# Kernel optimization log

Measured on AMD Instinct MI355X. Metric: run time of the kernel, lower is better.

## Reference

```python
import jax, jax.numpy as jnp
import numpy as np

SCALE = 256.0  # emulates SharedFxpShift = 8 fixed-point shift


def requant(x):
    # RequantFxpToScaledInt8: shift down by SharedFxpShift and clamp to int8 range
    return jnp.clip(x / SCALE, -128.0, 127.0)


def prelu(x, a):
    return jnp.where(x >= 0, x, a * x)


def _linearize(c):
    # injective encoding of 3D int coords (coords in [-8, 2040) after +8 shift)
    c = c.astype(jnp.int64) + 8
    B = 2048
    return (c[:, 0] * B + c[:, 1]) * B + c[:, 2]


def sparse_conv(coords, feats, W, stride):
    # 3x3x3 submanifold sparse conv: for each kernel offset, hash-lookup the
    # neighbor via sorted linearized coords + searchsorted, gather, matmul.
    # coords [N,3] int32, feats [N,Cin], W [27,Cin,Cout]
    lin = _linearize(coords)
    perm = jnp.argsort(lin)
    slin = lin[perm]
    N = coords.shape[0]
    out = jnp.zeros((N, W.shape[-1]), feats.dtype)
    k = 0
    for dx in (-1, 0, 1):
        for dy in (-1, 0, 1):
            for dz in (-1, 0, 1):
                off = jnp.array([dx, dy, dz], jnp.int32) * stride
                q = _linearize(coords + off[None, :])
                pos = jnp.clip(jnp.searchsorted(slin, q), 0, N - 1)
                hit = slin[pos] == q
                nb = perm[pos]
                f = jnp.where(hit[:, None], feats[nb], 0.0)
                out = out + f @ W[k]
                k += 1
    return out


def setup_inputs() -> dict:
    N, M, C = 200000, 400000, 64
    rng = np.random.default_rng(0)
    # unique parent coords: multiples of 2 in 512^3 grid
    lin = rng.choice(2 ** 24, size=N, replace=False).astype(np.int64)
    px = (lin // (256 * 256)) % 256
    py = (lin // 256) % 256
    pz = lin % 256
    rec_C = (np.stack([px, py, pz], 1) * 2).astype(np.int32)  # [N,3], stride 2
    # exactly M occupied children out of N*8, sorted (row-major mask order)
    child_idx = np.sort(rng.choice(N * 8, size=M, replace=False)).astype(np.int32)
    parent = child_idx // 8
    bit = child_idx % 8
    off = np.stack([(bit >> 2) & 1, (bit >> 1) & 1, bit & 1], 1).astype(np.int32)
    child_C = rec_C[parent] + off  # [M,3], stride 1, unique
    bins1_bits = np.zeros((N, 8), np.int32)
    bins1_bits[parent, bit] = 1
    bins0_bits = rng.integers(0, 2, size=(M, 8)).astype(np.int32)

    key = jax.random.key(0)
    ks = jax.random.split(key, 20)

    def w(k, shape, fan_in):
        return jax.random.normal(k, shape, jnp.float32) / np.sqrt(fan_in)

    inp = {
        "rec_F": jax.random.normal(ks[0], (N, C), jnp.float32) * SCALE,
        "dec_W": w(ks[1], (C + 8, C), C + 8),
        "dec_b": w(ks[2], (C,), 1) * 0.1,
        "dec_a": jnp.full((C,), 0.25, jnp.float32),
        "res_W1": w(ks[3], (27, C, C), 27 * C),
        "res_b1": w(ks[4], (C,), 1) * 0.1,
        "res_a1": jnp.full((C,), 0.25, jnp.float32),
        "res_W2": w(ks[5], (27, C, C), 27 * C),
        "res_b2": w(ks[6], (C,), 1) * 0.1,
        "p0_Wc": w(ks[7], (27, C, C), 27 * C),
        "p0_bc": w(ks[8], (C,), 1) * 0.1,
        "p0_ac": jnp.full((C,), 0.25, jnp.float32),
        "p0_Wl": w(ks[9], (C, C * 8), C),
        "p1_Wc": w(ks[10], (27, C, C), 27 * C),
        "p1_bc": w(ks[11], (C,), 1) * 0.1,
        "p1_ac": jnp.full((C,), 0.25, jnp.float32),
        "p1_Wl": w(ks[12], (C, 255), C),
        "rec_C": jnp.asarray(rec_C),
        "bins1_bits": jnp.asarray(bins1_bits),
        "child_idx": jnp.asarray(child_idx),
        "child_C": jnp.asarray(child_C),
        "bins0_bits": jnp.asarray(bins0_bits),
    }
    return inp


def reference(rec_F, dec_W, dec_b, dec_a, res_W1, res_b1, res_a1, res_W2, res_b2,
              p0_Wc, p0_bc, p0_ac, p0_Wl, p1_Wc, p1_bc, p1_ac, p1_Wl,
              rec_C, bins1_bits, child_idx, child_C, bins0_bits):
    C = dec_W.shape[1]
    # embed (empty Sequential for pred_steps=2): bins1.F << SharedFxpShift
    embed_f = bins1_bits.astype(jnp.float32) * SCALE  # [N,8]
    x = jnp.concatenate([rec_F, embed_f], 1)  # [N, C+8]
    # dec: Requant -> LinearPReLU(C+8 -> C, out32) -> ResBlock(C)
    h = requant(x)
    h = prelu(h @ dec_W + dec_b, dec_a)  # [N,C]
    r = requant(h)
    r = prelu(sparse_conv(rec_C, r, res_W1, 2) + res_b1, res_a1)
    r = requant(r)
    r = sparse_conv(rec_C, r, res_W2, 2) + res_b2
    rec_out = h + r  # [N,C]
    # pred[0]: Requant -> SparseConvPReLU(out8) -> Linear(C -> 8C, out32)
    p = requant(rec_out)
    p = requant(prelu(sparse_conv(rec_C, p, p0_Wc, 2) + p0_bc, p0_ac))
    p = p @ p0_Wl  # [N, 8C]
    # boolean-mask gather of occupied children: reshape [N,8,C] then mask ->
    # equals flat row gather with precomputed sorted child indices
    p = p.reshape(-1, C)[child_idx]  # [M,C]
    # pred[1] (last): Requant -> SparseConvPReLU(out8) -> Linear(C -> 255, out32)
    p = requant(p)
    p = requant(prelu(sparse_conv(child_C, p, p1_Wc, 1) + p1_bc, p1_ac))
    pred_out = p @ p1_Wl  # [M,255]
    # cur_oct = (cur_bins[0].F << bin2oct_kernel).sum(1) - 1
    k = jnp.arange(8, dtype=jnp.int32)
    cur_oct = ((bins0_bits << k).sum(1) - 1).astype(jnp.int16)  # [M]
    return rec_out, pred_out, cur_oct
```

## Files before the change

kernel.cpp:

```cpp
#include <hip/hip_runtime.h>
#include <stdint.h>


typedef short bf16x8 __attribute__((ext_vector_type(8)));
typedef float f32x4 __attribute__((ext_vector_type(4)));

#define EMPTY_KEY 0xFFFFFFFFu

__device__ __forceinline__ float rq(float x) {
  x *= (1.0f / 256.0f);
  return fminf(fmaxf(x, -128.0f), 127.0f);
}

__device__ __forceinline__ short f2b(float f) {
  union { float f; uint32_t u; } v; v.f = f;
  uint32_t u = v.u;
  uint32_t r = (u + 0x7FFFu + ((u >> 16) & 1u)) >> 16;
  return (short)r;
}

__device__ __forceinline__ uint32_t hkey(int x, int y, int z) {
  return ((uint32_t)(x + 8) << 20) | ((uint32_t)(y + 8) << 10) | (uint32_t)(z + 8);
}
__device__ __forceinline__ uint32_t hfun(uint32_t key, uint32_t mask) {
  return (key * 2654435761u) & mask;
}


__device__ __forceinline__ void pack_conv_elem(const float* __restrict__ W,
                                               short* __restrict__ dst, int gid) {
  int lane = gid & 63;
  int c = (gid >> 6) & 3;
  int t = (gid >> 8) & 1;
  int k = gid >> 9;
  int n = c * 16 + (lane & 15);
  int g = lane >> 4;
  bf16x8 v;
#pragma unroll
  for (int e = 0; e < 8; e++) {
    int kk = t * 32 + g * 8 + e;
    v[e] = f2b(W[(k * 64 + kk) * 64 + n]);
  }
  *(bf16x8*)(dst + gid * 8) = v;
}

__device__ __forceinline__ void pack_dense_elem(const float* __restrict__ W,
                                                short* __restrict__ dst, int K,
                                                int Ncols, int KT, int CT, int gid) {
  if (gid >= KT * CT * 64) return;
  int lane = gid & 63;
  int c = (gid >> 6) % CT;
  int t = gid / (64 * CT);
  int n = c * 16 + (lane & 15);
  int g = lane >> 4;
  bf16x8 v;
#pragma unroll
  for (int e = 0; e < 8; e++) {
    int kk = t * 32 + g * 8 + e;
    float val = (kk < K && n < Ncols) ? W[kk * Ncols + n] : 0.0f;
    v[e] = f2b(val);
  }
  *(bf16x8*)(dst + gid * 8) = v;
}

struct SetupA {
  const float *dec_W, *p0_Wl, *p1_Wl, *res_W1, *res_W2, *p0_Wc, *p1_Wc;
  const int *bins1, *child_idx, *bins0;
  uint32_t* rkeys;
  short *wpack, *decwp, *p0wp, *p1wp;
  int *bitsPk, *pStart, *bcnt;
  float* outOct;
  int N, M;
};

__global__ void __launch_bounds__(256) k_setupA(SetupA s) {
  int bid = blockIdx.x, tid = threadIdx.x;
  if (bid < 2048) {
    s.rkeys[bid * 256 + tid] = EMPTY_KEY;
    return;
  }
  bid -= 2048;
  if (bid < 216) {
    int which = bid / 54, sb = bid % 54;
    int gid = sb * 256 + tid;
    if (gid < 27 * 2 * 4 * 64) {
      const float* W = which == 0 ? s.res_W1 : which == 1 ? s.res_W2
                     : which == 2 ? s.p0_Wc : s.p1_Wc;
      pack_conv_elem(W, s.wpack + which * 110592, gid);
    }
    return;
  }
  bid -= 216;
  if (bid < 27) {
    if (bid < 3) pack_dense_elem(s.dec_W, s.decwp, 72, 64, 3, 4, bid * 256 + tid);
    else if (bid < 19) pack_dense_elem(s.p0_Wl, s.p0wp, 64, 512, 2, 32, (bid - 3) * 256 + tid);
    else pack_dense_elem(s.p1_Wl, s.p1wp, 64, 255, 2, 16, (bid - 19) * 256 + tid);
    return;
  }
  bid -= 27;
  int nbN = (s.N + 255) / 256, nbM = (s.M + 255) / 256;
  if (bid < nbN) {
    int p = bid * 256 + tid;
    if (p < s.N) {
      int b = 0;
#pragma unroll
      for (int e = 0; e < 8; e++) b |= (s.bins1[(size_t)p * 8 + e] & 1) << e;
      s.bitsPk[p] = b;
    }
    return;
  }
  bid -= nbN;
  if (bid < nbM) {
    int m = bid * 256 + tid;
    if (m < s.M) {
      int p = s.child_idx[m] >> 3;
      if (m == 0 || (s.child_idx[m - 1] >> 3) != p) s.pStart[p] = m;
    }
    return;
  }
  bid -= nbM;
  if (bid < nbM) {
    int m = bid * 256 + tid;
    if (m < s.M) {
      int ss = 0;
#pragma unroll
      for (int e = 0; e < 8; e++) ss += s.bins0[(size_t)m * 8 + e] << e;
      s.outOct[m] = (float)(ss - 1);
    }
    return;
  }
  if (tid < 8) s.bcnt[tid] = 0;
}

__global__ void __launch_bounds__(256)
k_setupB(const int* __restrict__ rec_C, const int* __restrict__ child_idx,
         uint32_t* __restrict__ rkeys, int* __restrict__ rvals,
         int* __restrict__ lists, int* __restrict__ cnt, int N, int M) {
  int bid = blockIdx.x, tid = threadIdx.x;
  int nbN = (N + 255) / 256;
  if (bid < nbN) {
    int i = bid * 256 + tid;
    if (i >= N) return;
    uint32_t key = hkey(rec_C[i * 3], rec_C[i * 3 + 1], rec_C[i * 3 + 2]);
    uint32_t s = hfun(key, (1u << 19) - 1);
    while (true) {
      uint32_t old = atomicCAS(&rkeys[s], EMPTY_KEY, key);
      if (old == EMPTY_KEY) { rvals[s] = i; return; }
      s = (s + 1) & ((1u << 19) - 1);
    }
  }
  bid -= nbN;
  __shared__ int lcnt[8];
  __shared__ int lbase[8];
  if (tid < 8) lcnt[tid] = 0;
  __syncthreads();
  int m = bid * 256 + tid;
  int b = 0, lp = 0;
  if (m < M) {
    b = child_idx[m] & 7;
    lp = atomicAdd(&lcnt[b], 1);
  }
  __syncthreads();
  if (tid < 8) lbase[tid] = atomicAdd(&cnt[tid], lcnt[tid]);
  __syncthreads();
  if (m < M) lists[(size_t)b * M + lbase[b] + lp] = m;
}

__global__ void __launch_bounds__(256)
k_setupC1(const int* __restrict__ rec_C,
          const uint32_t* __restrict__ rkeys, const int* __restrict__ rvals,
          int* __restrict__ nbrR, int N) {
  const uint32_t rmask = (1u << 19) - 1;
  int t = blockIdx.x * 256 + threadIdx.x;
  if (t >= N * 27) return;
  int i = t / 27, k = t % 27;
  int dx = k / 9 - 1, dy = (k / 3) % 3 - 1, dz = k % 3 - 1;
  int x = rec_C[i * 3] + dx * 2;
  int y = rec_C[i * 3 + 1] + dy * 2;
  int z = rec_C[i * 3 + 2] + dz * 2;
  uint32_t key = hkey(x, y, z);
  uint32_t s = hfun(key, rmask);
  int res = -1;
  while (true) {
    uint32_t kk = rkeys[s];
    if (kk == key) { res = rvals[s]; break; }
    if (kk == EMPTY_KEY) break;
    s = (s + 1) & rmask;
  }
  nbrR[(size_t)i * 28 + k] = res;
}

__global__ void __launch_bounds__(256)
k_setupC2(const int* __restrict__ child_C, const int* __restrict__ child_idx,
          const int* __restrict__ nbrR, const int* __restrict__ bitsPacked,
          const int* __restrict__ parentStart, int* __restrict__ nbrC, int M) {
  int m = blockIdx.x * 256 + threadIdx.x;
  if (m >= M) return;
  int cx = child_C[(size_t)m * 3], cy = child_C[(size_t)m * 3 + 1],
      cz = child_C[(size_t)m * 3 + 2];
  int pr = child_idx[m] >> 3;
  const int* nrow = nbrR + (size_t)pr * 28;
  int px = cx & 1, py = cy & 1, pz = cz & 1;

  int b8[8], s8[8];
#pragma unroll
  for (int j = 0; j < 8; j++) {
    int ddx = (px - 1) + ((j >> 2) & 1);
    int ddy = (py - 1) + ((j >> 1) & 1);
    int ddz = (pz - 1) + (j & 1);
    int kk = (ddx + 1) * 9 + (ddy + 1) * 3 + (ddz + 1);
    int r = nrow[kk];
    b8[j] = (r >= 0) ? bitsPacked[r] : 0;
    s8[j] = (r >= 0) ? parentStart[r] : 0;
  }

  int nout[28];
  nout[27] = -1;
#pragma unroll
  for (int k = 0; k < 27; k++) {
    const int dx = k / 9 - 1, dy = (k / 3) % 3 - 1, dz = k % 3 - 1;
    int tx = cx + dx, ty = cy + dy, tz = cz + dz;
    int jx = ((px + dx + 2) >> 1) - px;
    int jy = ((py + dy + 2) >> 1) - py;
    int jz = ((pz + dz + 2) >> 1) - pz;
    int j = jx * 4 + jy * 2 + jz;
    int bit = ((tx & 1) << 2) | ((ty & 1) << 1) | (tz & 1);
    int bits = b8[j];
    int res = -1;
    if ((bits >> bit) & 1) res = s8[j] + __popc(bits & ((1 << bit) - 1));
    nout[k] = res;
  }
#pragma unroll
  for (int q = 0; q < 7; q++)
    *(int4*)(nbrC + (size_t)m * 28 + q * 4) =
        make_int4(nout[q * 4], nout[q * 4 + 1], nout[q * 4 + 2], nout[q * 4 + 3]);
}


__global__ void __launch_bounds__(256)
k_dec(const float* __restrict__ recF, const int* __restrict__ bits,
      const short* __restrict__ wp, const float* __restrict__ bias,
      const float* __restrict__ alpha, float* __restrict__ h32,
      short* __restrict__ hq) {
  int tid = threadIdx.x, wid = tid >> 6, lane = tid & 63;
  int rowbase = blockIdx.x * 64 + wid * 16;
  int lrow = rowbase + (lane & 15);
  int g = lane >> 4;
  f32x4 acc[4] = {};
#pragma unroll
  for (int t = 0; t < 3; t++) {
    bf16x8 a = {0, 0, 0, 0, 0, 0, 0, 0};
    if (t < 2) {
      const float* src = recF + (size_t)lrow * 64 + t * 32 + g * 8;
#pragma unroll
      for (int e = 0; e < 8; e++) a[e] = f2b(rq(src[e]));
    } else if (g == 0) {
      const int* bp = bits + (size_t)lrow * 8;
#pragma unroll
      for (int e = 0; e < 8; e++) a[e] = f2b((float)bp[e]);
    }
#pragma unroll
    for (int c = 0; c < 4; c++) {
      bf16x8 b = *(const bf16x8*)(wp + ((t * 4 + c) * 64 + lane) * 8);
      acc[c] = __builtin_amdgcn_mfma_f32_16x16x32_bf16(a, b, acc[c], 0, 0, 0);
    }
  }
#pragma unroll
  for (int c = 0; c < 4; c++) {
    int col = c * 16 + (lane & 15);
    float bi = bias[col], al = alpha[col];
#pragma unroll
    for (int r = 0; r < 4; r++) {
      int row = rowbase + g * 4 + r;
      float v = acc[c][r] + bi;
      v = v >= 0.0f ? v : al * v;
      h32[(size_t)row * 64 + col] = v;
      hq[(size_t)row * 64 + col] = f2b(rq(v));
    }
  }
}

template <int MODE>
__global__ void __launch_bounds__(256)
k_conv(const short* __restrict__ fin, const int* __restrict__ nbr,
       const short* __restrict__ wp, const float* __restrict__ bias,
       const float* __restrict__ alpha, const float* __restrict__ resid,
       float* __restrict__ out32, short* __restrict__ outq) {
  int tid = threadIdx.x, wid = tid >> 6, lane = tid & 63;
  int rowbase = blockIdx.x * 64 + wid * 16;
  int lrow = rowbase + (lane & 15);
  int g = lane >> 4;

  int4 nv[7];
#pragma unroll
  for (int j = 0; j < 7; j++)
    nv[j] = *(const int4*)(nbr + (size_t)lrow * 28 + j * 4);
  int nbk[28];
#pragma unroll
  for (int j = 0; j < 7; j++) {
    nbk[j * 4 + 0] = nv[j].x;
    nbk[j * 4 + 1] = nv[j].y;
    nbk[j * 4 + 2] = nv[j].z;
    nbk[j * 4 + 3] = nv[j].w;
  }

  const bf16x8 zz = {0, 0, 0, 0, 0, 0, 0, 0};
  f32x4 acc[4] = {};
#pragma unroll
  for (int k = 0; k < 27; k++) {
    if (__any(nbk[k] >= 0)) {
      int nb = nbk[k];
      int safe = nb >= 0 ? nb : 0;
      const short* fp = fin + (size_t)safe * 64 + g * 8;
      bf16x8 a0 = *(const bf16x8*)fp;
      bf16x8 a1 = *(const bf16x8*)(fp + 32);
      a0 = nb >= 0 ? a0 : zz;
      a1 = nb >= 0 ? a1 : zz;
      const short* wk = wp + k * 4096;
#pragma unroll
      for (int c = 0; c < 4; c++) {
        bf16x8 b0 = *(const bf16x8*)(wk + (c * 64 + lane) * 8);
        acc[c] = __builtin_amdgcn_mfma_f32_16x16x32_bf16(a0, b0, acc[c], 0, 0, 0);
      }
#pragma unroll
      for (int c = 0; c < 4; c++) {
        bf16x8 b1 = *(const bf16x8*)(wk + ((4 + c) * 64 + lane) * 8);
        acc[c] = __builtin_amdgcn_mfma_f32_16x16x32_bf16(a1, b1, acc[c], 0, 0, 0);
      }
    }
  }
#pragma unroll
  for (int c = 0; c < 4; c++) {
    int col = c * 16 + (lane & 15);
    float bi = bias[col];
    float al = (MODE == 0) ? alpha[col] : 0.0f;
#pragma unroll
    for (int r = 0; r < 4; r++) {
      int row = rowbase + g * 4 + r;
      float v = acc[c][r] + bi;
      if (MODE == 0) {
        v = v >= 0.0f ? v : al * v;
        outq[(size_t)row * 64 + col] = f2b(rq(v));
      } else {
        v += resid[(size_t)row * 64 + col];
        out32[(size_t)row * 64 + col] = v;
        outq[(size_t)row * 64 + col] = f2b(rq(v));
      }
    }
  }
}

__global__ void __launch_bounds__(256)
k_p0(const short* __restrict__ qq, const int* __restrict__ child_idx,
     const int* __restrict__ lists, const int* __restrict__ cnt,
     const short* __restrict__ wp, short* __restrict__ tq, int M) {
  int b = blockIdx.y;
  int cb = cnt[b];
  int start = blockIdx.x * 64;
  if (start >= cb) return;
  int tid = threadIdx.x, wid = tid >> 6, lane = tid & 63, g = lane >> 4;
  int posA = start + wid * 16 + (lane & 15);
  int parent = -1;
  if (posA < cb) parent = child_idx[lists[(size_t)b * M + posA]] >> 3;
  f32x4 acc[4] = {};
#pragma unroll
  for (int t = 0; t < 2; t++) {
    bf16x8 a = {0, 0, 0, 0, 0, 0, 0, 0};
    if (parent >= 0) a = *(const bf16x8*)(qq + (size_t)parent * 64 + t * 32 + g * 8);
#pragma unroll
    for (int c = 0; c < 4; c++) {
      bf16x8 bb = *(const bf16x8*)(wp + (((size_t)t * 32 + b * 4 + c) * 64 + lane) * 8);
      acc[c] = __builtin_amdgcn_mfma_f32_16x16x32_bf16(a, bb, acc[c], 0, 0, 0);
    }
  }
#pragma unroll
  for (int r = 0; r < 4; r++) {
    int posD = start + wid * 16 + g * 4 + r;
    if (posD < cb) {
      int m = lists[(size_t)b * M + posD];
#pragma unroll
      for (int c = 0; c < 4; c++) {
        int col = c * 16 + (lane & 15);
        tq[(size_t)m * 64 + col] = f2b(rq(acc[c][r]));
      }
    }
  }
}

__global__ void __launch_bounds__(256, 4)
k_convp1(const short* __restrict__ fin, const int* __restrict__ nbr,
         const short* __restrict__ wp, const float* __restrict__ bias,
         const float* __restrict__ alpha,
         const int* __restrict__ lists, const int* __restrict__ cnt,
         const short* __restrict__ p1wp, float* __restrict__ out, int M) {
  __shared__ short lds[4][16][64];
  __shared__ int mrow[4][16];
  int b = blockIdx.y;
  int cb = cnt[b];
  int start = blockIdx.x * 64;
  if (start >= cb) return;
  int tid = threadIdx.x, wid = tid >> 6, lane = tid & 63;
  int l15 = lane & 15, g = lane >> 4;

  int pos = start + wid * 16 + l15;
  int m = (pos < cb) ? lists[(size_t)b * M + pos] : -1;
  if (g == 0) mrow[wid][l15] = m;

  int msafe = m >= 0 ? m : 0;
  const int* nrow = nbr + (size_t)msafe * 28;

  int px = (b >> 2) & 1, py = (b >> 1) & 1, pz = b & 1;
  int kown[8];
  uint32_t ownMask = 0;
#pragma unroll
  for (int j = 0; j < 8; j++) {
    int k = (((j >> 2) & 1) - px + 1) * 9 + (((j >> 1) & 1) - py + 1) * 3 +
            ((j & 1) - pz + 1);
    kown[j] = k;
    ownMask |= 1u << k;
  }

  int nbo[8];
#pragma unroll
  for (int j = 0; j < 8; j++) nbo[j] = nrow[kown[j]];
  int4 nv[7];
#pragma unroll
  for (int j = 0; j < 7; j++) nv[j] = *(const int4*)(nrow + j * 4);
  __builtin_amdgcn_sched_barrier(0);

  const bf16x8 zz = {0, 0, 0, 0, 0, 0, 0, 0};

  bf16x8 A0[8], A1[8];
#pragma unroll
  for (int j = 0; j < 8; j++) {
    int nb = (m >= 0) ? nbo[j] : -1;
    int safe = nb >= 0 ? nb : 0;
    const short* fp = fin + (size_t)safe * 64 + g * 8;
    bf16x8 x0 = *(const bf16x8*)fp;
    bf16x8 x1 = *(const bf16x8*)(fp + 32);
    A0[j] = nb >= 0 ? x0 : zz;
    A1[j] = nb >= 0 ? x1 : zz;
  }
  __builtin_amdgcn_sched_barrier(0);

  f32x4 acc[4] = {};
#pragma unroll
  for (int j = 0; j < 8; j++) {
    const short* wk = wp + kown[j] * 4096;
#pragma unroll
    for (int c = 0; c < 4; c++) {
      bf16x8 b0 = *(const bf16x8*)(wk + (c * 64 + lane) * 8);
      acc[c] = __builtin_amdgcn_mfma_f32_16x16x32_bf16(A0[j], b0, acc[c], 0, 0, 0);
    }
#pragma unroll
    for (int c = 0; c < 4; c++) {
      bf16x8 b1 = *(const bf16x8*)(wk + ((4 + c) * 64 + lane) * 8);
      acc[c] = __builtin_amdgcn_mfma_f32_16x16x32_bf16(A1[j], b1, acc[c], 0, 0, 0);
    }
  }

  int nbk[28];
#pragma unroll
  for (int j = 0; j < 7; j++) {
    nbk[j * 4 + 0] = m >= 0 ? nv[j].x : -1;
    nbk[j * 4 + 1] = m >= 0 ? nv[j].y : -1;
    nbk[j * 4 + 2] = m >= 0 ? nv[j].z : -1;
    nbk[j * 4 + 3] = m >= 0 ? nv[j].w : -1;
  }
#pragma unroll
  for (int k = 0; k < 27; k++) {
    if (!((ownMask >> k) & 1) && __any(nbk[k] >= 0)) {
      int nb = nbk[k];
      int safe = nb >= 0 ? nb : 0;
      const short* fp = fin + (size_t)safe * 64 + g * 8;
      bf16x8 a0 = *(const bf16x8*)fp;
      bf16x8 a1 = *(const bf16x8*)(fp + 32);
      a0 = nb >= 0 ? a0 : zz;
      a1 = nb >= 0 ? a1 : zz;
      const short* wk = wp + k * 4096;
#pragma unroll
      for (int c = 0; c < 4; c++) {
        bf16x8 b0 = *(const bf16x8*)(wk + (c * 64 + lane) * 8);
        acc[c] = __builtin_amdgcn_mfma_f32_16x16x32_bf16(a0, b0, acc[c], 0, 0, 0);
      }
#pragma unroll
      for (int c = 0; c < 4; c++) {
        bf16x8 b1 = *(const bf16x8*)(wk + ((4 + c) * 64 + lane) * 8);
        acc[c] = __builtin_amdgcn_mfma_f32_16x16x32_bf16(a1, b1, acc[c], 0, 0, 0);
      }
    }
  }

#pragma unroll
  for (int c = 0; c < 4; c++) {
    int col = c * 16 + l15;
    float bi = bias[col], al = alpha[col];
#pragma unroll
    for (int r = 0; r < 4; r++) {
      int rowW = g * 4 + r;
      float v = acc[c][r] + bi;
      v = v >= 0.0f ? v : al * v;
      lds[wid][rowW][col ^ ((rowW & 7) << 3)] = f2b(rq(v));
    }
  }
  __syncthreads();

  bf16x8 a0 = *(const bf16x8*)&lds[wid][l15][(g * 8) ^ ((l15 & 7) << 3)];
  bf16x8 a1 = *(const bf16x8*)&lds[wid][l15][(32 + g * 8) ^ ((l15 & 7) << 3)];
#pragma unroll
  for (int grp = 0; grp < 4; grp++) {
    f32x4 a2[4] = {};
#pragma unroll
    for (int c = 0; c < 4; c++) {
      bf16x8 b0 = *(const bf16x8*)(p1wp + ((grp * 4 + c) * 64 + lane) * 8);
      a2[c] = __builtin_amdgcn_mfma_f32_16x16x32_bf16(a0, b0, a2[c], 0, 0, 0);
      bf16x8 b1 = *(const bf16x8*)(p1wp + ((16 + grp * 4 + c) * 64 + lane) * 8);
      a2[c] = __builtin_amdgcn_mfma_f32_16x16x32_bf16(a1, b1, a2[c], 0, 0, 0);
    }
#pragma unroll
    for (int r = 0; r < 4; r++) {
      int mo = mrow[wid][g * 4 + r];
      if (mo >= 0) {
#pragma unroll
        for (int c = 0; c < 4; c++) {
          int col = (grp * 4 + c) * 16 + l15;
          if (col < 255) out[(size_t)mo * 255 + col] = a2[c][r];
        }
      }
    }
  }
}


extern "C" void kernel_launch(void* const* d_in, const int* in_sizes, int n_in,
                              void* d_out, int out_size, void* d_ws, size_t ws_size,
                              hipStream_t stream) {
  const float* rec_F  = (const float*)d_in[0];
  const float* dec_W  = (const float*)d_in[1];
  const float* dec_b  = (const float*)d_in[2];
  const float* dec_a  = (const float*)d_in[3];
  const float* res_W1 = (const float*)d_in[4];
  const float* res_b1 = (const float*)d_in[5];
  const float* res_a1 = (const float*)d_in[6];
  const float* res_W2 = (const float*)d_in[7];
  const float* res_b2 = (const float*)d_in[8];
  const float* p0_Wc  = (const float*)d_in[9];
  const float* p0_bc  = (const float*)d_in[10];
  const float* p0_ac  = (const float*)d_in[11];
  const float* p0_Wl  = (const float*)d_in[12];
  const float* p1_Wc  = (const float*)d_in[13];
  const float* p1_bc  = (const float*)d_in[14];
  const float* p1_ac  = (const float*)d_in[15];
  const float* p1_Wl  = (const float*)d_in[16];
  const int* rec_C    = (const int*)d_in[17];
  const int* bins1    = (const int*)d_in[18];
  const int* child_idx= (const int*)d_in[19];
  const int* child_C  = (const int*)d_in[20];
  const int* bins0    = (const int*)d_in[21];

  const int N = in_sizes[0] / 64;
  const int M = in_sizes[19];

  char* ws = (char*)d_ws;
  size_t off = 0;
  auto alloc = [&](size_t bytes) -> char* {
    char* p = ws + off;
    off += (bytes + 255) & ~(size_t)255;
    return p;
  };
  const uint32_t HR = 1u << 19;
  uint32_t* rkeys = (uint32_t*)alloc((size_t)HR * 4);
  int*      rvals = (int*)alloc((size_t)HR * 4);
  int* nbrR = (int*)alloc((size_t)N * 28 * 4);
  int* nbrC = (int*)alloc((size_t)M * 28 * 4);
  short* wpack = (short*)alloc((size_t)4 * 110592 * 2);
  short* decwp = (short*)alloc((size_t)3 * 4 * 64 * 8 * 2);
  short* p0wp  = (short*)alloc((size_t)2 * 32 * 64 * 8 * 2);
  short* p1wp  = (short*)alloc((size_t)2 * 16 * 64 * 8 * 2);
  short* bufA = (short*)alloc((size_t)N * 64 * 2);
  short* bufB = (short*)alloc((size_t)N * 64 * 2);
  float* h32  = (float*)alloc((size_t)N * 64 * 4);
  short* tq   = (short*)alloc((size_t)M * 64 * 2);
  int* lists  = (int*)alloc((size_t)8 * M * 4);
  int* bcnt   = (int*)alloc(256);
  int* bitsPk = (int*)alloc((size_t)N * 4);
  int* pStart = (int*)alloc((size_t)N * 4);

  float* outRec  = (float*)d_out;
  float* outPred = outRec + (size_t)N * 64;
  float* outOct  = outPred + (size_t)M * 255;

  dim3 B(256);
  int nbN = (N + 255) / 256, nbM = (M + 255) / 256;

  SetupA sa = {dec_W, p0_Wl, p1_Wl, res_W1, res_W2, p0_Wc, p1_Wc,
               bins1, child_idx, bins0, rkeys, wpack, decwp, p0wp, p1wp,
               bitsPk, pStart, bcnt, outOct, N, M};
  int gridA = 2048 + 216 + 27 + nbN + nbM + nbM + 1;
  k_setupA<<<gridA, B, 0, stream>>>(sa);
  k_setupB<<<nbN + nbM, B, 0, stream>>>(rec_C, child_idx, rkeys, rvals,
                                        lists, bcnt, N, M);
  k_setupC1<<<(N * 27 + 255) / 256, B, 0, stream>>>(rec_C, rkeys, rvals, nbrR, N);
  k_setupC2<<<nbM, B, 0, stream>>>(child_C, child_idx, nbrR, bitsPk, pStart,
                                   nbrC, M);

  k_dec<<<N / 64, B, 0, stream>>>(rec_F, bins1, decwp, dec_b, dec_a, h32, bufA);
  k_conv<0><<<N / 64, B, 0, stream>>>(bufA, nbrR, wpack, res_b1, res_a1,
                                      nullptr, nullptr, bufB);
  k_conv<1><<<N / 64, B, 0, stream>>>(bufB, nbrR, wpack + 110592, res_b2, nullptr,
                                      h32, outRec, bufA);
  k_conv<0><<<N / 64, B, 0, stream>>>(bufA, nbrR, wpack + 221184, p0_bc, p0_ac,
                                      nullptr, nullptr, bufB);
  k_p0<<<dim3(M / 64, 8), B, 0, stream>>>(bufB, child_idx, lists, bcnt, p0wp, tq, M);
  k_convp1<<<dim3((M + 63) / 64, 8), B, 0, stream>>>(
      tq, nbrC, wpack + 331776, p1_bc, p1_ac, lists, bcnt, p1wp, outPred, M);
}
```

Measured before the change: 602.8 us.

## Split final linear into separate kernel writing output rows contiguously

The fused p1 conv+linear kernel is split. The conv now writes bin-ordered bf16 activations to a compact buffer, and a new kernel does the 64->255 linear in output row order using an inverse permutation built at setup. Large fp32 output stores, which were scattered rows, become contiguous, which should improve write coalescing and locality. The cost is an extra M x 64 bf16 round trip, one more launch, and a gather in the new kernel.

```diff
diff --git a/kernel.cpp b/kernel.cpp
--- a/kernel.cpp
+++ b/kernel.cpp
@@ -164,6 +164,18 @@
   if (tid < 8) lbase[tid] = atomicAdd(&cnt[tid], lcnt[tid]);
   __syncthreads();
   if (m < M) lists[(size_t)b * M + lbase[b] + lp] = m;
+}
+
+__global__ void __launch_bounds__(256)
+k_invpos(const int* __restrict__ lists, const int* __restrict__ cnt,
+         int* __restrict__ invpos, int M) {
+  int b = blockIdx.y;
+  int pos = blockIdx.x * 256 + threadIdx.x;
+  if (pos >= cnt[b]) return;
+  int pref = 0;
+#pragma unroll
+  for (int i = 0; i < 8; i++) pref += (i < b) ? cnt[i] : 0;
+  invpos[lists[(size_t)b * M + pos]] = pref + pos;
 }
 
 __global__ void __launch_bounds__(256)
@@ -388,13 +400,12 @@
 }
 
 __global__ void __launch_bounds__(256, 4)
-k_convp1(const short* __restrict__ fin, const int* __restrict__ nbr,
-         const short* __restrict__ wp, const float* __restrict__ bias,
-         const float* __restrict__ alpha,
-         const int* __restrict__ lists, const int* __restrict__ cnt,
-         const short* __restrict__ p1wp, float* __restrict__ out, int M) {
+k_convu(const short* __restrict__ fin, const int* __restrict__ nbr,
+        const short* __restrict__ wp, const float* __restrict__ bias,
+        const float* __restrict__ alpha,
+        const int* __restrict__ lists, const int* __restrict__ cnt,
+        short* __restrict__ uq, int M) {
   __shared__ short lds[4][16][64];
-  __shared__ int mrow[4][16];
   int b = blockIdx.y;
   int cb = cnt[b];
   int start = blockIdx.x * 64;
@@ -404,7 +415,6 @@
 
   int pos = start + wid * 16 + l15;
   int m = (pos < cb) ? lists[(size_t)b * M + pos] : -1;
-  if (g == 0) mrow[wid][l15] = m;
 
   int msafe = m >= 0 ? m : 0;
   const int* nrow = nbr + (size_t)msafe * 28;
@@ -505,8 +515,29 @@
   }
   __syncthreads();
 
-  bf16x8 a0 = *(const bf16x8*)&lds[wid][l15][(g * 8) ^ ((l15 & 7) << 3)];
-  bf16x8 a1 = *(const bf16x8*)&lds[wid][l15][(32 + g * 8) ^ ((l15 & 7) << 3)];
+  int pref = 0;
+#pragma unroll
+  for (int i = 0; i < 8; i++) pref += (i < b) ? cnt[i] : 0;
+  if (pos < cb) {
+    size_t uqrow = (size_t)(pref + pos) * 64;
+    int swz = (l15 & 7) << 3;
+    bf16x8 c0 = *(const bf16x8*)&lds[wid][l15][(g * 8) ^ swz];
+    bf16x8 c1 = *(const bf16x8*)&lds[wid][l15][(32 + g * 8) ^ swz];
+    *(bf16x8*)(uq + uqrow + g * 8) = c0;
+    *(bf16x8*)(uq + uqrow + 32 + g * 8) = c1;
+  }
+}
+
+__global__ void __launch_bounds__(256, 4)
+k_p1(const short* __restrict__ uq, const int* __restrict__ invpos,
+     const short* __restrict__ p1wp, float* __restrict__ out) {
+  int tid = threadIdx.x, wid = tid >> 6, lane = tid & 63;
+  int l15 = lane & 15, g = lane >> 4;
+  int rowbase = blockIdx.x * 64 + wid * 16;
+  int lrow = rowbase + l15;
+  int gpos = invpos[lrow];
+  bf16x8 a0 = *(const bf16x8*)(uq + (size_t)gpos * 64 + g * 8);
+  bf16x8 a1 = *(const bf16x8*)(uq + (size_t)gpos * 64 + 32 + g * 8);
 #pragma unroll
   for (int grp = 0; grp < 4; grp++) {
     f32x4 a2[4] = {};
@@ -519,13 +550,11 @@
     }
 #pragma unroll
     for (int r = 0; r < 4; r++) {
-      int mo = mrow[wid][g * 4 + r];
-      if (mo >= 0) {
-#pragma unroll
-        for (int c = 0; c < 4; c++) {
-          int col = (grp * 4 + c) * 16 + l15;
-          if (col < 255) out[(size_t)mo * 255 + col] = a2[c][r];
-        }
+      int row = rowbase + g * 4 + r;
+#pragma unroll
+      for (int c = 0; c < 4; c++) {
+        int col = (grp * 4 + c) * 16 + l15;
+        if (col < 255) out[(size_t)row * 255 + col] = a2[c][r];
       }
     }
   }
@@ -581,10 +610,12 @@
   short* bufB = (short*)alloc((size_t)N * 64 * 2);
   float* h32  = (float*)alloc((size_t)N * 64 * 4);
   short* tq   = (short*)alloc((size_t)M * 64 * 2);
+  short* uq   = (short*)alloc((size_t)M * 64 * 2);
   int* lists  = (int*)alloc((size_t)8 * M * 4);
   int* bcnt   = (int*)alloc(256);
   int* bitsPk = (int*)alloc((size_t)N * 4);
   int* pStart = (int*)alloc((size_t)N * 4);
+  int* invpos = (int*)alloc((size_t)M * 4);
 
   float* outRec  = (float*)d_out;
   float* outPred = outRec + (size_t)N * 64;
@@ -600,6 +631,7 @@
   k_setupA<<<gridA, B, 0, stream>>>(sa);
   k_setupB<<<nbN + nbM, B, 0, stream>>>(rec_C, child_idx, rkeys, rvals,
                                         lists, bcnt, N, M);
+  k_invpos<<<dim3(nbM, 8), B, 0, stream>>>(lists, bcnt, invpos, M);
   k_setupC1<<<(N * 27 + 255) / 256, B, 0, stream>>>(rec_C, rkeys, rvals, nbrR, N);
   k_setupC2<<<nbM, B, 0, stream>>>(child_C, child_idx, nbrR, bitsPk, pStart,
                                    nbrC, M);
@@ -612,6 +644,7 @@
   k_conv<0><<<N / 64, B, 0, stream>>>(bufA, nbrR, wpack + 221184, p0_bc, p0_ac,
                                       nullptr, nullptr, bufB);
   k_p0<<<dim3(M / 64, 8), B, 0, stream>>>(bufB, child_idx, lists, bcnt, p0wp, tq, M);
-  k_convp1<<<dim3((M + 63) / 64, 8), B, 0, stream>>>(
-      tq, nbrC, wpack + 331776, p1_bc, p1_ac, lists, bcnt, p1wp, outPred, M);
-}
+  k_convu<<<dim3((M + 63) / 64, 8), B, 0, stream>>>(
+      tq, nbrC, wpack + 331776, p1_bc, p1_ac, lists, bcnt, uq, M);
+  k_p1<<<M / 64, B, 0, stream>>>(uq, invpos, p1wp, outPred);
+}
```

Result: no change. 614.2 us (+1.9%).
